# Kernel optimization log

Measured on AMD Instinct MI355X. Metric: run time of the kernel, lower is better.

The kernel has to match this reference:

```python
import jax, jax.numpy as jnp
import numpy as np

N_NODES = 100000


def gcn_conv(x, src, dst, W, b, n_nodes):
    """PyG GCNConv: add self-loops, symmetric deg^-1/2 normalization,
    linear transform, scatter-add aggregation, bias."""
    loop = jnp.arange(n_nodes, dtype=src.dtype)
    s = jnp.concatenate([src, loop])
    d = jnp.concatenate([dst, loop])
    # degree of destination nodes (includes self-loops)
    deg = jax.ops.segment_sum(jnp.ones(s.shape[0], dtype=x.dtype), d,
                              num_segments=n_nodes)
    dis = jnp.where(deg > 0, jax.lax.rsqrt(deg), 0.0)  # deg^-1/2
    norm = dis[s] * dis[d]                              # [E+N]
    h = x @ W                                           # [N, out]
    msg = h[s] * norm[:, None]                          # gather + scale
    out = jax.ops.segment_sum(msg, d, num_segments=n_nodes)  # scatter-add
    return out + b


def setup_inputs() -> dict:
    key = jax.random.key(0)
    k1, k2, k3, k4 = jax.random.split(key, 4)
    F_in, H, C = 500, 64, 10
    x = jax.random.normal(k1, (N_NODES, F_in), dtype=jnp.float32)
    edge_index = jax.random.randint(k2, (2, 1600000), 0, N_NODES,
                                    dtype=jnp.int32)
    W1 = jax.random.normal(k3, (F_in, H), dtype=jnp.float32) / np.sqrt(F_in)
    b1 = jnp.zeros((H,), dtype=jnp.float32)
    W2 = jax.random.normal(k4, (H, C), dtype=jnp.float32) / np.sqrt(H)
    b2 = jnp.zeros((C,), dtype=jnp.float32)
    return {"x": x, "edge_index": edge_index,
            "W1": W1, "b1": b1, "W2": W2, "b2": b2}


def reference(x, edge_index, W1, b1, W2, b2):
    src, dst = edge_index[0], edge_index[1]
    h = gcn_conv(x, src, dst, W1, b1, N_NODES)
    h = jax.nn.relu(h)
    # dropout is identity at inference (training=False)
    out = gcn_conv(h, src, dst, W2, b2, N_NODES)
    return out
```

## Files before the change

kernel.cpp:

```cpp
#include <hip/hip_runtime.h>

#define F_IN 500
#define HDIM 64
#define CDIM 10
#define KPAD 512
#define NSTAGE 16
#define H2LD 16

typedef __attribute__((ext_vector_type(8))) short bf16x8;
typedef __attribute__((ext_vector_type(4))) float floatx4;

__device__ inline unsigned short f2bf(float f) {
    unsigned int u = __float_as_uint(f);
    u += 0x7fffu + ((u >> 16) & 1u);
    return (unsigned short)(u >> 16);
}
__device__ inline float bflo(unsigned int u) { return __uint_as_float(u << 16); }
__device__ inline float bfhi(unsigned int u) { return __uint_as_float(u & 0xffff0000u); }

__global__ __launch_bounds__(256) void prep_kernel(
        const int* __restrict__ dst, int E, int* __restrict__ deg,
        int* __restrict__ erank,
        const float* __restrict__ W1, unsigned short* __restrict__ whf,
        unsigned short* __restrict__ wlf, int degB) {
    int bid = blockIdx.x;
    if (bid < degB) {
        int e = bid * 256 + threadIdx.x;
        if (e < E) erank[e] = atomicAdd(&deg[dst[e]], 1);
    } else {
        int idx = (bid - degB) * 256 + threadIdx.x;
        if (idx >= KPAD * HDIM) return;
        int k = idx >> 6;
        int f = idx & 63;
        float w = (k < F_IN) ? W1[k * HDIM + f] : 0.f;
        unsigned int b = __float_as_uint(w);
        unsigned short hh = (unsigned short)(b >> 16);
        float wl = w - __uint_as_float(b & 0xffff0000u);
        unsigned short ll = (unsigned short)(__float_as_uint(wl) >> 16);
        int kb = k >> 5, q = (k >> 3) & 3, j = k & 7;
        int fb = f >> 4, fl = f & 15;
        int lane = (q << 4) | fl;
        size_t o = ((((size_t)kb * 4 + fb) * 64 + lane) << 3) | (size_t)j;
        whf[o] = hh;
        wlf[o] = ll;
    }
}

__global__ void scan_block_kernel(const int* __restrict__ deg,
                                  int* __restrict__ row_ptr,
                                  int* __restrict__ blk_sum,
                                  float* __restrict__ dis, int Np1) {
    __shared__ int wsum[16];
    int i = blockIdx.x * 1024 + threadIdx.x;
    int v = (i < Np1 - 1) ? deg[i] : 0;
    if (i < Np1 - 1) dis[i] = rsqrtf((float)(v + 1));
    int lane = threadIdx.x & 63;
    int wid = threadIdx.x >> 6;
    int x = v;
#pragma unroll
    for (int off = 1; off < 64; off <<= 1) {
        int y = __shfl_up(x, off);
        if (lane >= off) x += y;
    }
    if (lane == 63) wsum[wid] = x;
    __syncthreads();
    if (threadIdx.x < 16) {
        int ws = wsum[threadIdx.x];
#pragma unroll
        for (int off = 1; off < 16; off <<= 1) {
            int y = __shfl_up(ws, off);
            if ((int)threadIdx.x >= off) ws += y;
        }
        wsum[threadIdx.x] = ws;
    }
    __syncthreads();
    int wp = (wid > 0) ? wsum[wid - 1] : 0;
    if (i < Np1) row_ptr[i] = wp + x - v;
    if (threadIdx.x == 1023) blk_sum[blockIdx.x] = wp + x;
}

__global__ void scan_top_kernel(int* __restrict__ blk_sum, int nb) {
    int carry = 0;
    for (int base = 0; base < nb; base += 64) {
        int i = base + (int)threadIdx.x;
        int v = (i < nb) ? blk_sum[i] : 0;
        int x = v;
#pragma unroll
        for (int off = 1; off < 64; off <<= 1) {
            int y = __shfl_up(x, off);
            if ((int)threadIdx.x >= off) x += y;
        }
        if (i < nb) blk_sum[i] = carry + x - v;
        carry += __shfl(x, 63);
    }
}

__global__ __launch_bounds__(256) void csr_gemm_kernel(
        const float* __restrict__ x, const unsigned short* __restrict__ whf,
        const unsigned short* __restrict__ wlf, const float* __restrict__ dis,
        unsigned short* __restrict__ h1b, int N,
        const int* __restrict__ src, const int* __restrict__ dst,
        const int* __restrict__ erank,
        const int* __restrict__ row_ptr, const int* __restrict__ blk_sum,
        int* __restrict__ csr_src, int E,
        int gemmB) {
    const int bid = blockIdx.x;
    const int g9 = bid / 9;
    const bool isGemm = (bid % 9 == 0) && (g9 < gemmB);
    if (!isGemm) {
        int before = (bid + 8) / 9;
        if (before > gemmB) before = gemmB;
        int cb = bid - before;
        int e = cb * 256 + threadIdx.x;
        if (e >= E) return;
        int d = dst[e];
        csr_src[row_ptr[d] + blk_sum[d >> 10] + erank[e]] = src[e];
        return;
    }
    const int lane = threadIdx.x & 63;
    const int wid = (g9 * 256 + threadIdx.x) >> 6;
    const int n0 = wid * 32;
    if (n0 >= N) return;
    const int q = lane >> 4;
    const int fl = lane & 15;

    int r0 = n0 + fl;       if (r0 >= N) r0 = N - 1;
    int r1 = n0 + 16 + fl;  if (r1 >= N) r1 = N - 1;
    const float* xp0 = x + (size_t)r0 * F_IN + q * 8;
    const float* xp1 = x + (size_t)r1 * F_IN + q * 8;

    floatx4 acc[2][4];
#pragma unroll
    for (int t = 0; t < 2; ++t)
#pragma unroll
        for (int fb = 0; fb < 4; ++fb) acc[t][fb] = (floatx4){0.f, 0.f, 0.f, 0.f};

    const bf16x8* whv = (const bf16x8*)whf;
    const bf16x8* wlv = (const bf16x8*)wlf;

    float4 na = *(const float4*)(xp0);
    float4 nb = *(const float4*)(xp0 + 4);
    float4 nc = *(const float4*)(xp1);
    float4 nd = *(const float4*)(xp1 + 4);

    for (int kb = 0; kb < NSTAGE - 1; ++kb) {
        float4 a = na, b = nb, c = nc, d = nd;
        if (kb + 1 < NSTAGE - 1) {
            na = *(const float4*)(xp0 + (kb + 1) * 32);
            nb = *(const float4*)(xp0 + (kb + 1) * 32 + 4);
            nc = *(const float4*)(xp1 + (kb + 1) * 32);
            nd = *(const float4*)(xp1 + (kb + 1) * 32 + 4);
        }
        float xv0[8] = {a.x, a.y, a.z, a.w, b.x, b.y, b.z, b.w};
        float xv1[8] = {c.x, c.y, c.z, c.w, d.x, d.y, d.z, d.w};
        bf16x8 xh0, xl0, xh1, xl1;
#pragma unroll
        for (int j = 0; j < 8; ++j) {
            unsigned int b0 = __float_as_uint(xv0[j]);
            xh0[j] = (short)(b0 >> 16);
            float res0 = xv0[j] - __uint_as_float(b0 & 0xffff0000u);
            xl0[j] = (short)(__float_as_uint(res0) >> 16);
            unsigned int b1 = __float_as_uint(xv1[j]);
            xh1[j] = (short)(b1 >> 16);
            float res1 = xv1[j] - __uint_as_float(b1 & 0xffff0000u);
            xl1[j] = (short)(__float_as_uint(res1) >> 16);
        }
#pragma unroll
        for (int fb = 0; fb < 4; ++fb) {
            bf16x8 bh = whv[(size_t)(kb * 4 + fb) * 64 + lane];
            bf16x8 bl = wlv[(size_t)(kb * 4 + fb) * 64 + lane];
            acc[0][fb] = __builtin_amdgcn_mfma_f32_16x16x32_bf16(xh0, bh, acc[0][fb], 0, 0, 0);
            acc[0][fb] = __builtin_amdgcn_mfma_f32_16x16x32_bf16(xl0, bh, acc[0][fb], 0, 0, 0);
            acc[0][fb] = __builtin_amdgcn_mfma_f32_16x16x32_bf16(xh0, bl, acc[0][fb], 0, 0, 0);
            acc[1][fb] = __builtin_amdgcn_mfma_f32_16x16x32_bf16(xh1, bh, acc[1][fb], 0, 0, 0);
            acc[1][fb] = __builtin_amdgcn_mfma_f32_16x16x32_bf16(xl1, bh, acc[1][fb], 0, 0, 0);
            acc[1][fb] = __builtin_amdgcn_mfma_f32_16x16x32_bf16(xh1, bl, acc[1][fb], 0, 0, 0);
        }
    }
    {
        const int kb = NSTAGE - 1;
        float xv0[8], xv1[8];
#pragma unroll
        for (int j = 0; j < 8; ++j) {
            int kk = kb * 32 + q * 8 + j;
            xv0[j] = (kk < F_IN) ? xp0[kb * 32 + j] : 0.f;
            xv1[j] = (kk < F_IN) ? xp1[kb * 32 + j] : 0.f;
        }
        bf16x8 xh0, xl0, xh1, xl1;
#pragma unroll
        for (int j = 0; j < 8; ++j) {
            unsigned int b0 = __float_as_uint(xv0[j]);
            xh0[j] = (short)(b0 >> 16);
            float res0 = xv0[j] - __uint_as_float(b0 & 0xffff0000u);
            xl0[j] = (short)(__float_as_uint(res0) >> 16);
            unsigned int b1 = __float_as_uint(xv1[j]);
            xh1[j] = (short)(b1 >> 16);
            float res1 = xv1[j] - __uint_as_float(b1 & 0xffff0000u);
            xl1[j] = (short)(__float_as_uint(res1) >> 16);
        }
#pragma unroll
        for (int fb = 0; fb < 4; ++fb) {
            bf16x8 bh = whv[(size_t)(kb * 4 + fb) * 64 + lane];
            bf16x8 bl = wlv[(size_t)(kb * 4 + fb) * 64 + lane];
            acc[0][fb] = __builtin_amdgcn_mfma_f32_16x16x32_bf16(xh0, bh, acc[0][fb], 0, 0, 0);
            acc[0][fb] = __builtin_amdgcn_mfma_f32_16x16x32_bf16(xl0, bh, acc[0][fb], 0, 0, 0);
            acc[0][fb] = __builtin_amdgcn_mfma_f32_16x16x32_bf16(xh0, bl, acc[0][fb], 0, 0, 0);
            acc[1][fb] = __builtin_amdgcn_mfma_f32_16x16x32_bf16(xh1, bh, acc[1][fb], 0, 0, 0);
            acc[1][fb] = __builtin_amdgcn_mfma_f32_16x16x32_bf16(xl1, bh, acc[1][fb], 0, 0, 0);
            acc[1][fb] = __builtin_amdgcn_mfma_f32_16x16x32_bf16(xh1, bl, acc[1][fb], 0, 0, 0);
        }
    }
#pragma unroll
    for (int t = 0; t < 2; ++t) {
#pragma unroll
        for (int r = 0; r < 4; ++r) {
            int node = n0 + t * 16 + q * 4 + r;
            if (node < N) {
                float dn = dis[node];
#pragma unroll
                for (int fb = 0; fb < 4; ++fb) {
                    h1b[(size_t)node * HDIM + fb * 16 + fl] =
                        f2bf(acc[t][fb][r] * dn);
                }
            }
        }
    }
}

__global__ __launch_bounds__(256) void gather1_kernel(
        const int* __restrict__ row_ptr, const int* __restrict__ blk_sum,
        const int* __restrict__ csr_src, const float* __restrict__ dis,
        const unsigned short* __restrict__ h1b,
        float* __restrict__ agg1, int N) {
    int nid = blockIdx.x * 4 + (threadIdx.x >> 6);
    if (nid >= N) return;
    int node = __builtin_amdgcn_readfirstlane(nid);
    int lane = threadIdx.x & 63;
    int half = lane >> 5;
    int c = lane & 31;
    int beg = row_ptr[node] + blk_sum[node >> 10];
    int end = row_ptr[node + 1] + blk_sum[(node + 1) >> 10];
    float dd = dis[node];
    float a0 = 0.f, a1 = 0.f;
    if (half == 0) {
        unsigned int w = *reinterpret_cast<const unsigned int*>(
            h1b + (size_t)node * HDIM + 2 * c);
        a0 = bflo(w);
        a1 = bfhi(w);
    }
    int p = beg + half;
    for (; p + 14 < end; p += 16) {
        unsigned int wv[8];
#pragma unroll
        for (int i = 0; i < 8; ++i) {
            int s = csr_src[p + 2 * i];
            wv[i] = *reinterpret_cast<const unsigned int*>(
                h1b + (size_t)s * HDIM + 2 * c);
        }
#pragma unroll
        for (int i = 0; i < 8; ++i) {
            a0 += bflo(wv[i]);
            a1 += bfhi(wv[i]);
        }
    }
    for (; p < end; p += 2) {
        int s0 = csr_src[p];
        unsigned int w0 = *reinterpret_cast<const unsigned int*>(
            h1b + (size_t)s0 * HDIM + 2 * c);
        a0 += bflo(w0);
        a1 += bfhi(w0);
    }
    a0 += __shfl_xor(a0, 32);
    a1 += __shfl_xor(a1, 32);
    if (half == 0) {
        *reinterpret_cast<float2*>(agg1 + (size_t)node * HDIM + 2 * c) =
            make_float2(a0 * dd, a1 * dd);
    }
}

__global__ void layer2_kernel(const float* __restrict__ agg1,
                              const float* __restrict__ b1,
                              const float* __restrict__ W2,
                              const float* __restrict__ dis,
                              float* __restrict__ h2s, int N) {
    int n = blockIdx.x * blockDim.x + threadIdx.x;
    if (n >= N) return;
    const float* ar = agg1 + (size_t)n * HDIM;
    float t[HDIM];
#pragma unroll
    for (int c = 0; c < HDIM; ++c) {
        float v = ar[c] + b1[c];
        t[c] = v > 0.f ? v : 0.f;
    }
    float dn = dis[n];
    float* h2r = h2s + (size_t)n * H2LD;
#pragma unroll
    for (int j = 0; j < CDIM; ++j) {
        float acc = 0.f;
#pragma unroll
        for (int c = 0; c < HDIM; ++c) acc = fmaf(t[c], W2[c * CDIM + j], acc);
        h2r[j] = acc * dn;
    }
}

__global__ __launch_bounds__(256) void gather2_kernel(
        const int* __restrict__ row_ptr, const int* __restrict__ blk_sum,
        const int* __restrict__ csr_src, const float* __restrict__ dis,
        const float* __restrict__ h2s, const float* __restrict__ b2,
        float* __restrict__ out, int N) {
    int nid = blockIdx.x * 4 + (threadIdx.x >> 6);
    if (nid >= N) return;
    int node = __builtin_amdgcn_readfirstlane(nid);
    int lane = threadIdx.x & 63;
    int g = lane >> 4;
    int j = lane & 15;
    int beg = row_ptr[node] + blk_sum[node >> 10];
    int end = row_ptr[node + 1] + blk_sum[(node + 1) >> 10];
    float acc = 0.f;
    int p = beg + g;
    for (; p + 12 < end; p += 16) {
        int s0 = csr_src[p];
        int s1 = csr_src[p + 4];
        int s2 = csr_src[p + 8];
        int s3 = csr_src[p + 12];
        float v0 = (j < CDIM) ? h2s[(size_t)s0 * H2LD + j] : 0.f;
        float v1 = (j < CDIM) ? h2s[(size_t)s1 * H2LD + j] : 0.f;
        float v2 = (j < CDIM) ? h2s[(size_t)s2 * H2LD + j] : 0.f;
        float v3 = (j < CDIM) ? h2s[(size_t)s3 * H2LD + j] : 0.f;
        acc += (v0 + v1) + (v2 + v3);
    }
    for (; p < end; p += 4) {
        int s0 = csr_src[p];
        acc += (j < CDIM) ? h2s[(size_t)s0 * H2LD + j] : 0.f;
    }
    acc += __shfl_xor(acc, 16);
    acc += __shfl_xor(acc, 32);
    if (lane < CDIM) {
        float dd = dis[node];
        out[(size_t)node * CDIM + lane] =
            b2[lane] + dd * (acc + h2s[(size_t)node * H2LD + lane]);
    }
}

static inline char* align256(char* p) {
    return (char*)(((uintptr_t)p + 255) & ~(uintptr_t)255);
}

extern "C" void kernel_launch(void* const* d_in, const int* in_sizes, int n_in,
                              void* d_out, int out_size, void* d_ws,
                              size_t ws_size, hipStream_t stream) {
    const float* x  = (const float*)d_in[0];
    const int*   ei = (const int*)d_in[1];
    const float* W1 = (const float*)d_in[2];
    const float* b1 = (const float*)d_in[3];
    const float* W2 = (const float*)d_in[4];
    const float* b2 = (const float*)d_in[5];

    const int N = in_sizes[0] / F_IN;
    const int E = in_sizes[1] / 2;
    const int* src = ei;
    const int* dst = ei + E;
    float* out = (float*)d_out;

    const int Np1 = N + 1;
    const int nscan_blocks = (Np1 + 1023) / 1024;

    char* w = (char*)d_ws;
    int* deg = (int*)w;                  w = align256(w + (size_t)N * 4);
    char* zero_end = w;
    int* erank = (int*)w;                w = align256(w + (size_t)E * 4);
    float* dis = (float*)w;              w = align256(w + (size_t)N * 4);
    int* row_ptr = (int*)w;              w = align256(w + (size_t)(N + 4) * 4);
    int* blk_sum = (int*)w;              w = align256(w + (size_t)nscan_blocks * 4);
    int* csr_src = (int*)w;              w = align256(w + (size_t)E * 4);
    unsigned short* whf = (unsigned short*)w;  w = align256(w + (size_t)KPAD * HDIM * 2);
    unsigned short* wlf = (unsigned short*)w;  w = align256(w + (size_t)KPAD * HDIM * 2);
    unsigned short* h1b = (unsigned short*)w;  w = align256(w + (size_t)N * HDIM * 2);
    float* agg1 = (float*)w;             w = align256(w + (size_t)N * HDIM * 4);
    float* h2s = (float*)w;              w = align256(w + (size_t)N * H2LD * 4);

    hipMemsetAsync(deg, 0, (size_t)(zero_end - (char*)deg), stream);

    const int degB = (E + 255) / 256;
    const int wprepB = (KPAD * HDIM + 255) / 256;
    prep_kernel<<<degB + wprepB, 256, 0, stream>>>(dst, E, deg, erank, W1, whf,
                                                   wlf, degB);
    scan_block_kernel<<<nscan_blocks, 1024, 0, stream>>>(deg, row_ptr, blk_sum,
                                                         dis, Np1);
    scan_top_kernel<<<1, 64, 0, stream>>>(blk_sum, nscan_blocks);
    {
        int gemmB = ((N + 31) / 32 + 3) / 4;
        int csrB = (E + 255) / 256;
        csr_gemm_kernel<<<gemmB + csrB, 256, 0, stream>>>(
            x, whf, wlf, dis, h1b, N,
            src, dst, erank, row_ptr, blk_sum, csr_src, E, gemmB);
    }
    gather1_kernel<<<(N + 3) / 4, 256, 0, stream>>>(row_ptr, blk_sum, csr_src,
                                                    dis, h1b, agg1, N);
    layer2_kernel<<<(N + 255) / 256, 256, 0, stream>>>(agg1, b1, W2, dis, h2s,
                                                       N);
    gather2_kernel<<<(N + 3) / 4, 256, 0, stream>>>(row_ptr, blk_sum, csr_src,
                                                    dis, h2s, b2, out, N);
}
```

Baseline: 543.5 us.

## Fuse layer-2 transform into gather1 and retile GEMM to 16 rows per wave

Removes the agg1 intermediate buffer and the separate layer2 kernel by applying bias, ReLU and the 64x10 W2 projection inside the gather1 wave, with wave shuffles doing the reduction. This avoids writing and re-reading a 100000x64 float array. The GEMM is also retiled so each wave handles 16 rows instead of 32, with deeper x prefetch and double-buffered weight registers, and GEMM blocks are interleaved 1 in 5 with the CSR-fill blocks. In exchange, each node now pays for many shuffles, and the row clamping at the N boundary was dropped, which relies on N being a multiple of 16.

```diff
diff --git a/kernel.cpp b/kernel.cpp
--- a/kernel.cpp
+++ b/kernel.cpp
@@ -17,6 +17,17 @@
 }
 __device__ inline float bflo(unsigned int u) { return __uint_as_float(u << 16); }
 __device__ inline float bfhi(unsigned int u) { return __uint_as_float(u & 0xffff0000u); }
+
+__device__ inline void split8(float4 a, float4 b, bf16x8& xh, bf16x8& xl) {
+    float xv[8] = {a.x, a.y, a.z, a.w, b.x, b.y, b.z, b.w};
+#pragma unroll
+    for (int j = 0; j < 8; ++j) {
+        unsigned int u = __float_as_uint(xv[j]);
+        xh[j] = (short)(u >> 16);
+        float r = xv[j] - __uint_as_float(u & 0xffff0000u);
+        xl[j] = (short)(__float_as_uint(r) >> 16);
+    }
+}
 
 __global__ __launch_bounds__(256) void prep_kernel(
         const int* __restrict__ dst, int E, int* __restrict__ deg,
@@ -105,10 +116,10 @@
         int* __restrict__ csr_src, int E,
         int gemmB) {
     const int bid = blockIdx.x;
-    const int g9 = bid / 9;
-    const bool isGemm = (bid % 9 == 0) && (g9 < gemmB);
+    const int g5 = bid / 5;
+    const bool isGemm = (bid % 5 == 0) && (g5 < gemmB);
     if (!isGemm) {
-        int before = (bid + 8) / 9;
+        int before = (bid + 4) / 5;
         if (before > gemmB) before = gemmB;
         int cb = bid - before;
         int e = cb * 256 + threadIdx.x;
@@ -118,120 +129,102 @@
         return;
     }
     const int lane = threadIdx.x & 63;
-    const int wid = (g9 * 256 + threadIdx.x) >> 6;
-    const int n0 = wid * 32;
+    const int wid = (g5 << 2) + (threadIdx.x >> 6);
+    const int n0 = wid * 16;
     if (n0 >= N) return;
     const int q = lane >> 4;
     const int fl = lane & 15;
-
-    int r0 = n0 + fl;       if (r0 >= N) r0 = N - 1;
-    int r1 = n0 + 16 + fl;  if (r1 >= N) r1 = N - 1;
-    const float* xp0 = x + (size_t)r0 * F_IN + q * 8;
-    const float* xp1 = x + (size_t)r1 * F_IN + q * 8;
-
-    floatx4 acc[2][4];
-#pragma unroll
-    for (int t = 0; t < 2; ++t)
-#pragma unroll
-        for (int fb = 0; fb < 4; ++fb) acc[t][fb] = (floatx4){0.f, 0.f, 0.f, 0.f};
+    const float* xp = x + (size_t)(n0 + fl) * F_IN + q * 8;
 
     const bf16x8* whv = (const bf16x8*)whf;
     const bf16x8* wlv = (const bf16x8*)wlf;
 
-    float4 na = *(const float4*)(xp0);
-    float4 nb = *(const float4*)(xp0 + 4);
-    float4 nc = *(const float4*)(xp1);
-    float4 nd = *(const float4*)(xp1 + 4);
-
+    floatx4 acc[4];
+#pragma unroll
+    for (int fb = 0; fb < 4; ++fb) acc[fb] = (floatx4){0.f, 0.f, 0.f, 0.f};
+
+    float4 xa[4], xb[4];
+    bf16x8 wh[2][4], wl[2][4];
+
+    xa[0] = *(const float4*)(xp);
+    xb[0] = *(const float4*)(xp + 4);
+    xa[1] = *(const float4*)(xp + 32);
+    xb[1] = *(const float4*)(xp + 36);
+    xa[2] = *(const float4*)(xp + 64);
+    xb[2] = *(const float4*)(xp + 68);
+#pragma unroll
+    for (int fb = 0; fb < 4; ++fb) {
+        wh[0][fb] = whv[(size_t)fb * 64 + lane];
+        wl[0][fb] = wlv[(size_t)fb * 64 + lane];
+    }
+
+#pragma unroll
     for (int kb = 0; kb < NSTAGE - 1; ++kb) {
-        float4 a = na, b = nb, c = nc, d = nd;
-        if (kb + 1 < NSTAGE - 1) {
-            na = *(const float4*)(xp0 + (kb + 1) * 32);
-            nb = *(const float4*)(xp0 + (kb + 1) * 32 + 4);
-            nc = *(const float4*)(xp1 + (kb + 1) * 32);
-            nd = *(const float4*)(xp1 + (kb + 1) * 32 + 4);
-        }
-        float xv0[8] = {a.x, a.y, a.z, a.w, b.x, b.y, b.z, b.w};
-        float xv1[8] = {c.x, c.y, c.z, c.w, d.x, d.y, d.z, d.w};
-        bf16x8 xh0, xl0, xh1, xl1;
-#pragma unroll
-        for (int j = 0; j < 8; ++j) {
-            unsigned int b0 = __float_as_uint(xv0[j]);
-            xh0[j] = (short)(b0 >> 16);
-            float res0 = xv0[j] - __uint_as_float(b0 & 0xffff0000u);
-            xl0[j] = (short)(__float_as_uint(res0) >> 16);
-            unsigned int b1 = __float_as_uint(xv1[j]);
-            xh1[j] = (short)(b1 >> 16);
-            float res1 = xv1[j] - __uint_as_float(b1 & 0xffff0000u);
-            xl1[j] = (short)(__float_as_uint(res1) >> 16);
-        }
+        const int cw = kb & 1, nw = cw ^ 1;
 #pragma unroll
         for (int fb = 0; fb < 4; ++fb) {
-            bf16x8 bh = whv[(size_t)(kb * 4 + fb) * 64 + lane];
-            bf16x8 bl = wlv[(size_t)(kb * 4 + fb) * 64 + lane];
-            acc[0][fb] = __builtin_amdgcn_mfma_f32_16x16x32_bf16(xh0, bh, acc[0][fb], 0, 0, 0);
-            acc[0][fb] = __builtin_amdgcn_mfma_f32_16x16x32_bf16(xl0, bh, acc[0][fb], 0, 0, 0);
-            acc[0][fb] = __builtin_amdgcn_mfma_f32_16x16x32_bf16(xh0, bl, acc[0][fb], 0, 0, 0);
-            acc[1][fb] = __builtin_amdgcn_mfma_f32_16x16x32_bf16(xh1, bh, acc[1][fb], 0, 0, 0);
-            acc[1][fb] = __builtin_amdgcn_mfma_f32_16x16x32_bf16(xl1, bh, acc[1][fb], 0, 0, 0);
-            acc[1][fb] = __builtin_amdgcn_mfma_f32_16x16x32_bf16(xh1, bl, acc[1][fb], 0, 0, 0);
+            wh[nw][fb] = whv[(size_t)((kb + 1) * 4 + fb) * 64 + lane];
+            wl[nw][fb] = wlv[(size_t)((kb + 1) * 4 + fb) * 64 + lane];
+        }
+        if (kb + 3 < NSTAGE - 1) {
+            xa[(kb + 3) & 3] = *(const float4*)(xp + (kb + 3) * 32);
+            xb[(kb + 3) & 3] = *(const float4*)(xp + (kb + 3) * 32 + 4);
+        }
+        bf16x8 xh, xl;
+        split8(xa[kb & 3], xb[kb & 3], xh, xl);
+#pragma unroll
+        for (int fb = 0; fb < 4; ++fb) {
+            acc[fb] = __builtin_amdgcn_mfma_f32_16x16x32_bf16(xh, wh[cw][fb], acc[fb], 0, 0, 0);
+            acc[fb] = __builtin_amdgcn_mfma_f32_16x16x32_bf16(xl, wh[cw][fb], acc[fb], 0, 0, 0);
+            acc[fb] = __builtin_amdgcn_mfma_f32_16x16x32_bf16(xh, wl[cw][fb], acc[fb], 0, 0, 0);
         }
     }
     {
         const int kb = NSTAGE - 1;
-        float xv0[8], xv1[8];
+        float xv[8];
 #pragma unroll
         for (int j = 0; j < 8; ++j) {
             int kk = kb * 32 + q * 8 + j;
-            xv0[j] = (kk < F_IN) ? xp0[kb * 32 + j] : 0.f;
-            xv1[j] = (kk < F_IN) ? xp1[kb * 32 + j] : 0.f;
-        }
-        bf16x8 xh0, xl0, xh1, xl1;
+            xv[j] = (kk < F_IN) ? xp[kb * 32 + j] : 0.f;
+        }
+        bf16x8 xh, xl;
 #pragma unroll
         for (int j = 0; j < 8; ++j) {
-            unsigned int b0 = __float_as_uint(xv0[j]);
-            xh0[j] = (short)(b0 >> 16);
-            float res0 = xv0[j] - __uint_as_float(b0 & 0xffff0000u);
-            xl0[j] = (short)(__float_as_uint(res0) >> 16);
-            unsigned int b1 = __float_as_uint(xv1[j]);
-            xh1[j] = (short)(b1 >> 16);
-            float res1 = xv1[j] - __uint_as_float(b1 & 0xffff0000u);
-            xl1[j] = (short)(__float_as_uint(res1) >> 16);
-        }
+            unsigned int u = __float_as_uint(xv[j]);
+            xh[j] = (short)(u >> 16);
+            float r = xv[j] - __uint_as_float(u & 0xffff0000u);
+            xl[j] = (short)(__float_as_uint(r) >> 16);
+        }
+        const int cw = kb & 1;
 #pragma unroll
         for (int fb = 0; fb < 4; ++fb) {
-            bf16x8 bh = whv[(size_t)(kb * 4 + fb) * 64 + lane];
-            bf16x8 bl = wlv[(size_t)(kb * 4 + fb) * 64 + lane];
-            acc[0][fb] = __builtin_amdgcn_mfma_f32_16x16x32_bf16(xh0, bh, acc[0][fb], 0, 0, 0);
-            acc[0][fb] = __builtin_amdgcn_mfma_f32_16x16x32_bf16(xl0, bh, acc[0][fb], 0, 0, 0);
-            acc[0][fb] = __builtin_amdgcn_mfma_f32_16x16x32_bf16(xh0, bl, acc[0][fb], 0, 0, 0);
-            acc[1][fb] = __builtin_amdgcn_mfma_f32_16x16x32_bf16(xh1, bh, acc[1][fb], 0, 0, 0);
-            acc[1][fb] = __builtin_amdgcn_mfma_f32_16x16x32_bf16(xl1, bh, acc[1][fb], 0, 0, 0);
-            acc[1][fb] = __builtin_amdgcn_mfma_f32_16x16x32_bf16(xh1, bl, acc[1][fb], 0, 0, 0);
-        }
-    }
-#pragma unroll
-    for (int t = 0; t < 2; ++t) {
-#pragma unroll
-        for (int r = 0; r < 4; ++r) {
-            int node = n0 + t * 16 + q * 4 + r;
-            if (node < N) {
-                float dn = dis[node];
-#pragma unroll
-                for (int fb = 0; fb < 4; ++fb) {
-                    h1b[(size_t)node * HDIM + fb * 16 + fl] =
-                        f2bf(acc[t][fb][r] * dn);
-                }
-            }
-        }
-    }
-}
-
-__global__ __launch_bounds__(256) void gather1_kernel(
+            acc[fb] = __builtin_amdgcn_mfma_f32_16x16x32_bf16(xh, wh[cw][fb], acc[fb], 0, 0, 0);
+            acc[fb] = __builtin_amdgcn_mfma_f32_16x16x32_bf16(xl, wh[cw][fb], acc[fb], 0, 0, 0);
+            acc[fb] = __builtin_amdgcn_mfma_f32_16x16x32_bf16(xh, wl[cw][fb], acc[fb], 0, 0, 0);
+        }
+    }
+#pragma unroll
+    for (int r = 0; r < 4; ++r) {
+        int node = n0 + q * 4 + r;
+        float dn = dis[node];
+#pragma unroll
+        for (int fb = 0; fb < 4; ++fb) {
+            h1b[(size_t)node * HDIM + fb * 16 + fl] = f2bf(acc[fb][r] * dn);
+        }
+    }
+}
+
+__global__ __launch_bounds__(256) void gather1_l2_kernel(
         const int* __restrict__ row_ptr, const int* __restrict__ blk_sum,
         const int* __restrict__ csr_src, const float* __restrict__ dis,
         const unsigned short* __restrict__ h1b,
-        float* __restrict__ agg1, int N) {
+        const float* __restrict__ b1, const float* __restrict__ W2,
+        float* __restrict__ h2s, int N) {
+    __shared__ float sW2[HDIM * CDIM];
+    __shared__ float sB1[HDIM];
+    for (int i = threadIdx.x; i < HDIM * CDIM; i += 256) sW2[i] = W2[i];
+    if (threadIdx.x < HDIM) sB1[threadIdx.x] = b1[threadIdx.x];
+    __syncthreads();
     int nid = blockIdx.x * 4 + (threadIdx.x >> 6);
     if (nid >= N) return;
     int node = __builtin_amdgcn_readfirstlane(nid);
@@ -272,34 +265,25 @@
     }
     a0 += __shfl_xor(a0, 32);
     a1 += __shfl_xor(a1, 32);
-    if (half == 0) {
-        *reinterpret_cast<float2*>(agg1 + (size_t)node * HDIM + 2 * c) =
-            make_float2(a0 * dd, a1 * dd);
-    }
-}
-
-__global__ void layer2_kernel(const float* __restrict__ agg1,
-                              const float* __restrict__ b1,
-                              const float* __restrict__ W2,
-                              const float* __restrict__ dis,
-                              float* __restrict__ h2s, int N) {
-    int n = blockIdx.x * blockDim.x + threadIdx.x;
-    if (n >= N) return;
-    const float* ar = agg1 + (size_t)n * HDIM;
-    float t[HDIM];
-#pragma unroll
-    for (int c = 0; c < HDIM; ++c) {
-        float v = ar[c] + b1[c];
-        t[c] = v > 0.f ? v : 0.f;
-    }
-    float dn = dis[n];
-    float* h2r = h2s + (size_t)n * H2LD;
-#pragma unroll
-    for (int j = 0; j < CDIM; ++j) {
-        float acc = 0.f;
-#pragma unroll
-        for (int c = 0; c < HDIM; ++c) acc = fmaf(t[c], W2[c * CDIM + j], acc);
-        h2r[j] = acc * dn;
+    float t0 = a0 * dd + sB1[2 * c];
+    float t1 = a1 * dd + sB1[2 * c + 1];
+    t0 = t0 > 0.f ? t0 : 0.f;
+    t1 = t1 > 0.f ? t1 : 0.f;
+    float pj[CDIM];
+#pragma unroll
+    for (int j = 0; j < CDIM; ++j)
+        pj[j] = t0 * sW2[(2 * c) * CDIM + j] + t1 * sW2[(2 * c + 1) * CDIM + j];
+#pragma unroll
+    for (int off = 1; off < 32; off <<= 1) {
+#pragma unroll
+        for (int j = 0; j < CDIM; ++j) pj[j] += __shfl_xor(pj[j], off);
+    }
+    if (lane < CDIM) {
+        float v = pj[0];
+#pragma unroll
+        for (int j = 1; j < CDIM; ++j)
+            if (lane == j) v = pj[j];
+        h2s[(size_t)node * H2LD + lane] = v * dd;
     }
 }
 
@@ -376,7 +360,6 @@
     unsigned short* whf = (unsigned short*)w;  w = align256(w + (size_t)KPAD * HDIM * 2);
     unsigned short* wlf = (unsigned short*)w;  w = align256(w + (size_t)KPAD * HDIM * 2);
     unsigned short* h1b = (unsigned short*)w;  w = align256(w + (size_t)N * HDIM * 2);
-    float* agg1 = (float*)w;             w = align256(w + (size_t)N * HDIM * 4);
     float* h2s = (float*)w;              w = align256(w + (size_t)N * H2LD * 4);
 
     hipMemsetAsync(deg, 0, (size_t)(zero_end - (char*)deg), stream);
@@ -389,16 +372,15 @@
                                                          dis, Np1);
     scan_top_kernel<<<1, 64, 0, stream>>>(blk_sum, nscan_blocks);
     {
-        int gemmB = ((N + 31) / 32 + 3) / 4;
+        int gemmB = ((N + 15) / 16 + 3) / 4;
         int csrB = (E + 255) / 256;
         csr_gemm_kernel<<<gemmB + csrB, 256, 0, stream>>>(
             x, whf, wlf, dis, h1b, N,
             src, dst, erank, row_ptr, blk_sum, csr_src, E, gemmB);
     }
-    gather1_kernel<<<(N + 3) / 4, 256, 0, stream>>>(row_ptr, blk_sum, csr_src,
-                                                    dis, h1b, agg1, N);
-    layer2_kernel<<<(N + 255) / 256, 256, 0, stream>>>(agg1, b1, W2, dis, h2s,
-                                                       N);
+    gather1_l2_kernel<<<(N + 3) / 4, 256, 0, stream>>>(row_ptr, blk_sum,
+                                                       csr_src, dis, h1b,
+                                                       b1, W2, h2s, N);
     gather2_kernel<<<(N + 3) / 4, 256, 0, stream>>>(row_ptr, blk_sum, csr_src,
                                                     dis, h2s, b2, out, N);
 }
```

After: 587.1 us. 8.0% more time.
